# Kernel optimization log

Hardware: AMD Instinct MI355X
Metric: run time of the kernel (lower is better)

Reference implementation:

```python
import jax, jax.numpy as jnp
import numpy as np

N, E, D = 10000, 320000, 256


def setup_inputs() -> dict:
    key = jax.random.key(0)
    ks = jax.random.split(key, 6)
    return {
        "event_emb": jax.random.normal(ks[0], (N, D), jnp.float32),
        "edge_index": jax.random.randint(ks[1], (2, E), 0, N),
        # GCNConv params (weight [D,D] + bias)
        "W1": jax.random.normal(ks[2], (D, D), jnp.float32) / np.sqrt(D).astype(np.float32),
        "b1": jnp.zeros((D,), jnp.float32),
        # GATConv params (shared lin for src/dst when in==out, heads=1, concat=False)
        "W2": jax.random.normal(ks[3], (D, D), jnp.float32) / np.sqrt(D).astype(np.float32),
        "att_src": jax.random.normal(ks[4], (D,), jnp.float32) / np.sqrt(D).astype(np.float32),
        "att_dst": jax.random.normal(ks[5], (D,), jnp.float32) / np.sqrt(D).astype(np.float32),
        "b2": jnp.zeros((D,), jnp.float32),
    }


def _add_self_loops(src, dst, n):
    loop = jnp.arange(n, dtype=src.dtype)
    return jnp.concatenate([src, loop]), jnp.concatenate([dst, loop])


def _gcn_conv(x, W, b, src, dst, n):
    # PyG GCNConv: D^{-1/2} (A+I) D^{-1/2} X W + b ; self-loops already in src/dst
    xw = x @ W  # [N, D]
    deg = jax.ops.segment_sum(jnp.ones(src.shape[0], x.dtype), dst, num_segments=n)
    dinv = jnp.where(deg > 0, jax.lax.rsqrt(deg), 0.0)
    norm = dinv[src] * dinv[dst]  # [E+N]
    agg = jax.ops.segment_sum(xw[src] * norm[:, None], dst, num_segments=n)
    return agg + b


def _gat_conv(x, W, a_src, a_dst, b, src, dst, n):
    # PyG GATConv heads=1, concat=False, negative_slope=0.2, add_self_loops=True
    xw = x @ W  # [N, D]
    e = jax.nn.leaky_relu((xw @ a_src)[src] + (xw @ a_dst)[dst], 0.2)  # [E+N]
    # softmax over incoming edges of each destination node
    m = jax.ops.segment_max(e, dst, num_segments=n)
    ex = jnp.exp(e - m[dst])
    s = jax.ops.segment_sum(ex, dst, num_segments=n)
    alpha = ex / (s[dst] + 1e-16)
    agg = jax.ops.segment_sum(alpha[:, None] * xw[src], dst, num_segments=n)
    return agg + b


def reference(event_emb, edge_index, W1, b1, W2, att_src, att_dst, b2):
    n = event_emb.shape[0]
    src, dst = _add_self_loops(edge_index[0], edge_index[1], n)
    x = jax.nn.relu(_gcn_conv(event_emb, W1, b1, src, dst, n))
    x = jax.nn.relu(_gat_conv(x, W2, att_src, att_dst, b2, src, dst, n))
    return x
```

## Files before the change

kernel.cpp:

```cpp
#include <hip/hip_runtime.h>
#include <hip/hip_fp16.h>

#define D 256
#define UN 8
#define CAP 64

typedef __attribute__((ext_vector_type(4))) _Float16 half4v;

__device__ __forceinline__ float leaky(float x) { return x > 0.f ? x : 0.2f * x; }

__global__ void fill_direct(const int* __restrict__ src, const int* __restrict__ dst, int E,
                            int* __restrict__ cnt, int* __restrict__ csr) {
    int e = blockIdx.x * blockDim.x + threadIdx.x;
    if (e < E) {
        int d = dst[e];
        int pos = atomicAdd(&cnt[d], 1);
        if (pos < CAP) csr[d * CAP + pos] = src[e];
    }
}

__global__ void gemm1_pre(const float* __restrict__ A, const float* __restrict__ B,
                          const int* __restrict__ cnt, _Float16* __restrict__ C, int M) {
    __shared__ float As[16][64];
    __shared__ float Bs[16][64];
    int t = threadIdx.x;
    int tx = t & 15, ty = t >> 4;
    int m0 = blockIdx.x << 6;
    int n0 = blockIdx.y << 6;
    int ar = t >> 2;
    int ak = (t & 3) << 2;
    int br = t >> 4;
    int bc = (t & 15) << 2;
    int arow = m0 + ar;
    if (arow >= M) arow = M - 1;
    float acc[4][4] = {};
    for (int k0 = 0; k0 < D; k0 += 16) {
        float4 av = *(const float4*)(A + (size_t)arow * D + k0 + ak);
        float4 bv = *(const float4*)(B + (size_t)(k0 + br) * D + n0 + bc);
        __syncthreads();
        As[ak + 0][ar] = av.x;
        As[ak + 1][ar] = av.y;
        As[ak + 2][ar] = av.z;
        As[ak + 3][ar] = av.w;
        *(float4*)(&Bs[br][bc]) = bv;
        __syncthreads();
#pragma unroll
        for (int kk = 0; kk < 16; kk++) {
            float4 a = *(const float4*)(&As[kk][ty << 2]);
            float4 b = *(const float4*)(&Bs[kk][tx << 2]);
            acc[0][0] += a.x * b.x; acc[0][1] += a.x * b.y; acc[0][2] += a.x * b.z; acc[0][3] += a.x * b.w;
            acc[1][0] += a.y * b.x; acc[1][1] += a.y * b.y; acc[1][2] += a.y * b.z; acc[1][3] += a.y * b.w;
            acc[2][0] += a.z * b.x; acc[2][1] += a.z * b.y; acc[2][2] += a.z * b.z; acc[2][3] += a.z * b.w;
            acc[3][0] += a.w * b.x; acc[3][1] += a.w * b.y; acc[3][2] += a.w * b.z; acc[3][3] += a.w * b.w;
        }
    }
#pragma unroll
    for (int i = 0; i < 4; i++) {
        int m = m0 + (ty << 2) + i;
        if (m < M) {
            float sc = rsqrtf((float)cnt[m] + 1.0f);
            half4v v = {(_Float16)(acc[i][0] * sc), (_Float16)(acc[i][1] * sc),
                        (_Float16)(acc[i][2] * sc), (_Float16)(acc[i][3] * sc)};
            *(half4v*)(C + (size_t)m * D + n0 + (tx << 2)) = v;
        }
    }
}

__global__ void gemm2_att(const float* __restrict__ A, const float* __restrict__ B,
                          const float* __restrict__ atS, const float* __restrict__ atD,
                          float* __restrict__ asrc, float* __restrict__ adst,
                          _Float16* __restrict__ C, int M) {
    __shared__ float As[16][64];
    __shared__ float Bs[16][64];
    int t = threadIdx.x;
    int tx = t & 15, ty = t >> 4;
    int m0 = blockIdx.x << 6;
    int n0 = blockIdx.y << 6;
    int ar = t >> 2;
    int ak = (t & 3) << 2;
    int br = t >> 4;
    int bc = (t & 15) << 2;
    int arow = m0 + ar;
    if (arow >= M) arow = M - 1;
    float acc[4][4] = {};
    for (int k0 = 0; k0 < D; k0 += 16) {
        float4 av = *(const float4*)(A + (size_t)arow * D + k0 + ak);
        float4 bv = *(const float4*)(B + (size_t)(k0 + br) * D + n0 + bc);
        __syncthreads();
        As[ak + 0][ar] = av.x;
        As[ak + 1][ar] = av.y;
        As[ak + 2][ar] = av.z;
        As[ak + 3][ar] = av.w;
        *(float4*)(&Bs[br][bc]) = bv;
        __syncthreads();
#pragma unroll
        for (int kk = 0; kk < 16; kk++) {
            float4 a = *(const float4*)(&As[kk][ty << 2]);
            float4 b = *(const float4*)(&Bs[kk][tx << 2]);
            acc[0][0] += a.x * b.x; acc[0][1] += a.x * b.y; acc[0][2] += a.x * b.z; acc[0][3] += a.x * b.w;
            acc[1][0] += a.y * b.x; acc[1][1] += a.y * b.y; acc[1][2] += a.y * b.z; acc[1][3] += a.y * b.w;
            acc[2][0] += a.z * b.x; acc[2][1] += a.z * b.y; acc[2][2] += a.z * b.z; acc[2][3] += a.z * b.w;
            acc[3][0] += a.w * b.x; acc[3][1] += a.w * b.y; acc[3][2] += a.w * b.z; acc[3][3] += a.w * b.w;
        }
    }
    float4 as4 = *(const float4*)(atS + n0 + (tx << 2));
    float4 ad4 = *(const float4*)(atD + n0 + (tx << 2));
#pragma unroll
    for (int i = 0; i < 4; i++) {
        int m = m0 + (ty << 2) + i;
        float ps = acc[i][0] * as4.x + acc[i][1] * as4.y + acc[i][2] * as4.z + acc[i][3] * as4.w;
        float pd = acc[i][0] * ad4.x + acc[i][1] * ad4.y + acc[i][2] * ad4.z + acc[i][3] * ad4.w;
#pragma unroll
        for (int off = 1; off < 16; off <<= 1) {
            ps += __shfl_xor(ps, off);
            pd += __shfl_xor(pd, off);
        }
        if (m < M) {
            half4v v = {(_Float16)acc[i][0], (_Float16)acc[i][1],
                        (_Float16)acc[i][2], (_Float16)acc[i][3]};
            *(half4v*)(C + (size_t)m * D + n0 + (tx << 2)) = v;
            if (tx == 0) {
                atomicAdd(&asrc[m], ps);
                atomicAdd(&adst[m], pd);
            }
        }
    }
}

__global__ void gcn_agg(const _Float16* __restrict__ xw1h, const int* __restrict__ csr,
                        const int* __restrict__ cnt, const float* __restrict__ b1,
                        float* __restrict__ x1, int n) {
    int node = (blockIdx.x << 2) + (threadIdx.x >> 6);
    if (node >= n) return;
    int lane = threadIdx.x & 63;
    float ax[UN][4];
#pragma unroll
    for (int j = 0; j < UN; j++) { ax[j][0] = ax[j][1] = ax[j][2] = ax[j][3] = 0.f; }
    {
        half4v v = ((const half4v*)(xw1h + (size_t)node * D))[lane];
        ax[0][0] = (float)v[0]; ax[0][1] = (float)v[1];
        ax[0][2] = (float)v[2]; ax[0][3] = (float)v[3];
    }
    int c = cnt[node];
    int deg = c < CAP ? c : CAP;
    int beg = node * CAP, end = beg + deg;
    int e = beg;
    for (; e + UN <= end; e += UN) {
        int s[UN];
#pragma unroll
        for (int j = 0; j < UN; j++) s[j] = csr[e + j];
#pragma unroll
        for (int j = 0; j < UN; j++) {
            half4v u = ((const half4v*)(xw1h + (size_t)s[j] * D))[lane];
            ax[j][0] += (float)u[0]; ax[j][1] += (float)u[1];
            ax[j][2] += (float)u[2]; ax[j][3] += (float)u[3];
        }
    }
    for (; e < end; e++) {
        int s = csr[e];
        half4v u = ((const half4v*)(xw1h + (size_t)s * D))[lane];
        ax[0][0] += (float)u[0]; ax[0][1] += (float)u[1];
        ax[0][2] += (float)u[2]; ax[0][3] += (float)u[3];
    }
    float a0 = 0.f, a1 = 0.f, a2 = 0.f, a3 = 0.f;
#pragma unroll
    for (int j = 0; j < UN; j++) { a0 += ax[j][0]; a1 += ax[j][1]; a2 += ax[j][2]; a3 += ax[j][3]; }
    float dd = rsqrtf((float)c + 1.0f);
    int c4 = lane * 4;
    float4 bb = *(const float4*)(b1 + c4);
    a0 = a0 * dd + bb.x; a1 = a1 * dd + bb.y; a2 = a2 * dd + bb.z; a3 = a3 * dd + bb.w;
    a0 = a0 > 0.f ? a0 : 0.f;
    a1 = a1 > 0.f ? a1 : 0.f;
    a2 = a2 > 0.f ? a2 : 0.f;
    a3 = a3 > 0.f ? a3 : 0.f;
    *(float4*)(x1 + (size_t)node * D + c4) = make_float4(a0, a1, a2, a3);
}

__global__ void gat_agg(const _Float16* __restrict__ xw2, const int* __restrict__ csr,
                        const int* __restrict__ cnt, const float* __restrict__ asrc,
                        const float* __restrict__ adst, const float* __restrict__ b2,
                        float* __restrict__ out, int n) {
    int node = (blockIdx.x << 2) + (threadIdx.x >> 6);
    if (node >= n) return;
    int lane = threadIdx.x & 63;
    float ad = adst[node];
    float e_self = leaky(asrc[node] + ad);
    float mj[UN], sj[UN], aj[UN][4];
#pragma unroll
    for (int j = 0; j < UN; j++) {
        mj[j] = -1e30f; sj[j] = 0.f;
        aj[j][0] = aj[j][1] = aj[j][2] = aj[j][3] = 0.f;
    }
    {
        half4v v = ((const half4v*)(xw2 + (size_t)node * D))[lane];
        mj[0] = e_self; sj[0] = 1.0f;
        aj[0][0] = (float)v[0]; aj[0][1] = (float)v[1];
        aj[0][2] = (float)v[2]; aj[0][3] = (float)v[3];
    }
    int c = cnt[node];
    int deg = c < CAP ? c : CAP;
    int beg = node * CAP, end = beg + deg;
    int e = beg;
    for (; e + UN <= end; e += UN) {
        int s[UN];
        float ev[UN];
#pragma unroll
        for (int j = 0; j < UN; j++) s[j] = csr[e + j];
#pragma unroll
        for (int j = 0; j < UN; j++) ev[j] = leaky(asrc[s[j]] + ad);
#pragma unroll
        for (int j = 0; j < UN; j++) {
            half4v u = ((const half4v*)(xw2 + (size_t)s[j] * D))[lane];
            float nm = mj[j] > ev[j] ? mj[j] : ev[j];
            float f = __expf(mj[j] - nm);
            float w = __expf(ev[j] - nm);
            mj[j] = nm;
            sj[j] = sj[j] * f + w;
            aj[j][0] = aj[j][0] * f + (float)u[0] * w;
            aj[j][1] = aj[j][1] * f + (float)u[1] * w;
            aj[j][2] = aj[j][2] * f + (float)u[2] * w;
            aj[j][3] = aj[j][3] * f + (float)u[3] * w;
        }
    }
    for (; e < end; e++) {
        int s = csr[e];
        float ev = leaky(asrc[s] + ad);
        half4v u = ((const half4v*)(xw2 + (size_t)s * D))[lane];
        float nm = mj[0] > ev ? mj[0] : ev;
        float f = __expf(mj[0] - nm);
        float w = __expf(ev - nm);
        mj[0] = nm;
        sj[0] = sj[0] * f + w;
        aj[0][0] = aj[0][0] * f + (float)u[0] * w;
        aj[0][1] = aj[0][1] * f + (float)u[1] * w;
        aj[0][2] = aj[0][2] * f + (float)u[2] * w;
        aj[0][3] = aj[0][3] * f + (float)u[3] * w;
    }
    float M = mj[0];
#pragma unroll
    for (int j = 1; j < UN; j++) M = M > mj[j] ? M : mj[j];
    float a0 = 0.f, a1 = 0.f, a2 = 0.f, a3 = 0.f, ssum = 0.f;
#pragma unroll
    for (int j = 0; j < UN; j++) {
        float f = __expf(mj[j] - M);
        ssum += sj[j] * f;
        a0 += aj[j][0] * f; a1 += aj[j][1] * f;
        a2 += aj[j][2] * f; a3 += aj[j][3] * f;
    }
    float inv = 1.0f / (ssum + 1e-16f);
    int c4 = lane * 4;
    float4 bb = *(const float4*)(b2 + c4);
    float r0 = a0 * inv + bb.x;
    float r1 = a1 * inv + bb.y;
    float r2 = a2 * inv + bb.z;
    float r3 = a3 * inv + bb.w;
    r0 = r0 > 0.f ? r0 : 0.f;
    r1 = r1 > 0.f ? r1 : 0.f;
    r2 = r2 > 0.f ? r2 : 0.f;
    r3 = r3 > 0.f ? r3 : 0.f;
    *(float4*)(out + (size_t)node * D + c4) = make_float4(r0, r1, r2, r3);
}


extern "C" void kernel_launch(void* const* d_in, const int* in_sizes, int n_in,
                              void* d_out, int out_size, void* d_ws, size_t ws_size,
                              hipStream_t stream) {
    const float* emb = (const float*)d_in[0];
    const int*   ei  = (const int*)d_in[1];
    const float* W1  = (const float*)d_in[2];
    const float* b1  = (const float*)d_in[3];
    const float* W2  = (const float*)d_in[4];
    const float* atS = (const float*)d_in[5];
    const float* atD = (const float*)d_in[6];
    const float* b2  = (const float*)d_in[7];

    int n = in_sizes[0] / D;
    int E = in_sizes[1] / 2;
    const int* src = ei;
    const int* dst = ei + E;

    char* w = (char*)d_ws;
    auto alloc = [&](size_t bytes) -> char* {
        char* p = w;
        w += (bytes + 255) & ~(size_t)255;
        return p;
    };
    int*      cnt  = (int*)alloc((size_t)n * 12);
    float*    asrc = (float*)(cnt + n);
    float*    adst = asrc + n;
    int*      csr  = (int*)alloc((size_t)n * CAP * 4);
    _Float16* xw1h = (_Float16*)alloc((size_t)n * D * 2);
    float*    x1   = (float*)alloc((size_t)n * D * 4);
    _Float16* xw2h = xw1h;

    hipMemsetAsync(cnt, 0, (size_t)n * 12, stream);

    int eb = (E + 255) / 256;
    fill_direct<<<eb, 256, 0, stream>>>(src, dst, E, cnt, csr);

    dim3 ggrid((n + 63) / 64, 4);
    gemm1_pre<<<ggrid, 256, 0, stream>>>(emb, W1, cnt, xw1h, n);

    int nb = (n + 3) / 4;
    gcn_agg<<<nb, 256, 0, stream>>>(xw1h, csr, cnt, b1, x1, n);

    gemm2_att<<<ggrid, 256, 0, stream>>>(x1, W2, atS, atD, asrc, adst, xw2h, n);

    gat_agg<<<nb, 256, 0, stream>>>(xw2h, csr, cnt, asrc, adst, b2, (float*)d_out, n);
}
```

Before: 199.9 us.

## Fuse all GNN stages into one cooperative persistent kernel with grid syncs

Replaces the memset and five separate launches with one cooperative kernel. It zeroes the counters, builds the CSR, and runs both GEMMs and both aggregations as grid-stride loops over tiles and node groups, with grid.sync between phases. The aim is to remove per-launch overhead and the gaps between kernels. In exchange, each phase runs on a persistent grid capped at 1024 blocks, which may reduce latency hiding in the gather stages, and each grid barrier has its own cost. The original multi-kernel path stays as a fallback if the cooperative launch fails.

Result: slower. 537.0 us (+168.6%).

```diff
diff --git a/kernel.cpp b/kernel.cpp
--- a/kernel.cpp
+++ b/kernel.cpp
@@ -1,5 +1,8 @@
 #include <hip/hip_runtime.h>
 #include <hip/hip_fp16.h>
+#include <hip/hip_cooperative_groups.h>
+
+namespace cg = cooperative_groups;
 
 #define D 256
 #define UN 8
@@ -9,28 +12,16 @@
 
 __device__ __forceinline__ float leaky(float x) { return x > 0.f ? x : 0.2f * x; }
 
-__global__ void fill_direct(const int* __restrict__ src, const int* __restrict__ dst, int E,
-                            int* __restrict__ cnt, int* __restrict__ csr) {
-    int e = blockIdx.x * blockDim.x + threadIdx.x;
-    if (e < E) {
-        int d = dst[e];
-        int pos = atomicAdd(&cnt[d], 1);
-        if (pos < CAP) csr[d * CAP + pos] = src[e];
-    }
-}
-
-__global__ void gemm1_pre(const float* __restrict__ A, const float* __restrict__ B,
-                          const int* __restrict__ cnt, _Float16* __restrict__ C, int M) {
+
+__device__ void gemm1_tile(const float* __restrict__ A, const float* __restrict__ B,
+                           const int* __restrict__ cnt, _Float16* __restrict__ C,
+                           int M, int bx, int by) {
     __shared__ float As[16][64];
     __shared__ float Bs[16][64];
     int t = threadIdx.x;
     int tx = t & 15, ty = t >> 4;
-    int m0 = blockIdx.x << 6;
-    int n0 = blockIdx.y << 6;
-    int ar = t >> 2;
-    int ak = (t & 3) << 2;
-    int br = t >> 4;
-    int bc = (t & 15) << 2;
+    int m0 = bx << 6, n0 = by << 6;
+    int ar = t >> 2, ak = (t & 3) << 2, br = t >> 4, bc = (t & 15) << 2;
     int arow = m0 + ar;
     if (arow >= M) arow = M - 1;
     float acc[4][4] = {};
@@ -66,20 +57,16 @@
     }
 }
 
-__global__ void gemm2_att(const float* __restrict__ A, const float* __restrict__ B,
-                          const float* __restrict__ atS, const float* __restrict__ atD,
-                          float* __restrict__ asrc, float* __restrict__ adst,
-                          _Float16* __restrict__ C, int M) {
+__device__ void gemm2_tile(const float* __restrict__ A, const float* __restrict__ B,
+                           const float* __restrict__ atS, const float* __restrict__ atD,
+                           float* __restrict__ asrc, float* __restrict__ adst,
+                           _Float16* __restrict__ C, int M, int bx, int by) {
     __shared__ float As[16][64];
     __shared__ float Bs[16][64];
     int t = threadIdx.x;
     int tx = t & 15, ty = t >> 4;
-    int m0 = blockIdx.x << 6;
-    int n0 = blockIdx.y << 6;
-    int ar = t >> 2;
-    int ak = (t & 3) << 2;
-    int br = t >> 4;
-    int bc = (t & 15) << 2;
+    int m0 = bx << 6, n0 = by << 6;
+    int ar = t >> 2, ak = (t & 3) << 2, br = t >> 4, bc = (t & 15) << 2;
     int arow = m0 + ar;
     if (arow >= M) arow = M - 1;
     float acc[4][4] = {};
@@ -127,10 +114,10 @@
     }
 }
 
-__global__ void gcn_agg(const _Float16* __restrict__ xw1h, const int* __restrict__ csr,
-                        const int* __restrict__ cnt, const float* __restrict__ b1,
-                        float* __restrict__ x1, int n) {
-    int node = (blockIdx.x << 2) + (threadIdx.x >> 6);
+__device__ void gcn_group(const _Float16* __restrict__ xw1h, const int* __restrict__ csr,
+                          const int* __restrict__ cnt, const float* __restrict__ b1,
+                          float* __restrict__ x1, int n, int g) {
+    int node = (g << 2) + (threadIdx.x >> 6);
     if (node >= n) return;
     int lane = threadIdx.x & 63;
     float ax[UN][4];
@@ -176,11 +163,11 @@
     *(float4*)(x1 + (size_t)node * D + c4) = make_float4(a0, a1, a2, a3);
 }
 
-__global__ void gat_agg(const _Float16* __restrict__ xw2, const int* __restrict__ csr,
-                        const int* __restrict__ cnt, const float* __restrict__ asrc,
-                        const float* __restrict__ adst, const float* __restrict__ b2,
-                        float* __restrict__ out, int n) {
-    int node = (blockIdx.x << 2) + (threadIdx.x >> 6);
+__device__ void gat_group(const _Float16* __restrict__ xw2, const int* __restrict__ csr,
+                          const int* __restrict__ cnt, const float* __restrict__ asrc,
+                          const float* __restrict__ adst, const float* __restrict__ b2,
+                          float* __restrict__ out, int n, int g) {
+    int node = (g << 2) + (threadIdx.x >> 6);
     if (node >= n) return;
     int lane = threadIdx.x & 63;
     float ad = adst[node];
@@ -261,6 +248,80 @@
     *(float4*)(out + (size_t)node * D + c4) = make_float4(r0, r1, r2, r3);
 }
 
+__global__ __launch_bounds__(256, 4) void fused_all(
+    const float* __restrict__ emb, const int* __restrict__ src, const int* __restrict__ dst,
+    const float* __restrict__ W1, const float* __restrict__ b1, const float* __restrict__ W2,
+    const float* __restrict__ atS, const float* __restrict__ atD, const float* __restrict__ b2,
+    int* cnt, float* asrc, float* adst, int* csr,
+    _Float16* xw1h, float* x1, float* out, int n, int E) {
+    cg::grid_group grid = cg::this_grid();
+    const int nb = gridDim.x;
+    const int tid = blockIdx.x * 256 + threadIdx.x;
+    const int nthr = nb * 256;
+
+    for (int i = tid; i < 3 * n; i += nthr) cnt[i] = 0;
+    grid.sync();
+
+    for (int e = tid; e < E; e += nthr) {
+        int d = dst[e];
+        int pos = atomicAdd(&cnt[d], 1);
+        if (pos < CAP) csr[d * CAP + pos] = src[e];
+    }
+    grid.sync();
+
+    {
+        int tiles = ((n + 63) >> 6) * 4;
+        for (int tl = blockIdx.x; tl < tiles; tl += nb)
+            gemm1_tile(emb, W1, cnt, xw1h, n, tl >> 2, tl & 3);
+    }
+    grid.sync();
+
+    {
+        int groups = (n + 3) >> 2;
+        for (int g = blockIdx.x; g < groups; g += nb)
+            gcn_group(xw1h, csr, cnt, b1, x1, n, g);
+    }
+    grid.sync();
+
+    {
+        int tiles = ((n + 63) >> 6) * 4;
+        for (int tl = blockIdx.x; tl < tiles; tl += nb)
+            gemm2_tile(x1, W2, atS, atD, asrc, adst, xw1h, n, tl >> 2, tl & 3);
+    }
+    grid.sync();
+
+    {
+        int groups = (n + 3) >> 2;
+        for (int g = blockIdx.x; g < groups; g += nb)
+            gat_group(xw1h, csr, cnt, asrc, adst, b2, out, n, g);
+    }
+}
+
+__global__ void k_fill(const int* __restrict__ src, const int* __restrict__ dst, int E,
+                       int* __restrict__ cnt, int* __restrict__ csr) {
+    int e = blockIdx.x * blockDim.x + threadIdx.x;
+    if (e < E) {
+        int d = dst[e];
+        int pos = atomicAdd(&cnt[d], 1);
+        if (pos < CAP) csr[d * CAP + pos] = src[e];
+    }
+}
+__global__ void k_gemm1(const float* A, const float* B, const int* cnt, _Float16* C, int M) {
+    gemm1_tile(A, B, cnt, C, M, blockIdx.x, blockIdx.y);
+}
+__global__ void k_gcn(const _Float16* xw1h, const int* csr, const int* cnt,
+                      const float* b1, float* x1, int n) {
+    gcn_group(xw1h, csr, cnt, b1, x1, n, blockIdx.x);
+}
+__global__ void k_gemm2(const float* A, const float* B, const float* atS, const float* atD,
+                        float* asrc, float* adst, _Float16* C, int M) {
+    gemm2_tile(A, B, atS, atD, asrc, adst, C, M, blockIdx.x, blockIdx.y);
+}
+__global__ void k_gat(const _Float16* xw2, const int* csr, const int* cnt, const float* asrc,
+                      const float* adst, const float* b2, float* out, int n) {
+    gat_group(xw2, csr, cnt, asrc, adst, b2, out, n, blockIdx.x);
+}
+
 
 extern "C" void kernel_launch(void* const* d_in, const int* in_sizes, int n_in,
                               void* d_out, int out_size, void* d_ws, size_t ws_size,
@@ -291,20 +352,35 @@
     int*      csr  = (int*)alloc((size_t)n * CAP * 4);
     _Float16* xw1h = (_Float16*)alloc((size_t)n * D * 2);
     float*    x1   = (float*)alloc((size_t)n * D * 4);
-    _Float16* xw2h = xw1h;
-
-    hipMemsetAsync(cnt, 0, (size_t)n * 12, stream);
-
-    int eb = (E + 255) / 256;
-    fill_direct<<<eb, 256, 0, stream>>>(src, dst, E, cnt, csr);
-
-    dim3 ggrid((n + 63) / 64, 4);
-    gemm1_pre<<<ggrid, 256, 0, stream>>>(emb, W1, cnt, xw1h, n);
-
-    int nb = (n + 3) / 4;
-    gcn_agg<<<nb, 256, 0, stream>>>(xw1h, csr, cnt, b1, x1, n);
-
-    gemm2_att<<<ggrid, 256, 0, stream>>>(x1, W2, atS, atD, asrc, adst, xw2h, n);
-
-    gat_agg<<<nb, 256, 0, stream>>>(xw2h, csr, cnt, asrc, adst, b2, (float*)d_out, n);
-}
+    float*    outp = (float*)d_out;
+
+    int dev = 0;
+    hipGetDevice(&dev);
+    int ncu = 0;
+    hipDeviceGetAttribute(&ncu, hipDeviceAttributeMultiprocessorCount, dev);
+    int maxb = 0;
+    hipOccupancyMaxActiveBlocksPerMultiprocessor(&maxb, fused_all, 256, 0);
+    long capb = (long)maxb * (long)ncu;
+    int grid = (capb < 1) ? 0 : (int)(capb < 1024 ? capb : 1024);
+
+    hipError_t rc = hipErrorUnknown;
+    if (grid > 0) {
+        void* args[] = {(void*)&emb, (void*)&src, (void*)&dst, (void*)&W1, (void*)&b1,
+                        (void*)&W2, (void*)&atS, (void*)&atD, (void*)&b2,
+                        (void*)&cnt, (void*)&asrc, (void*)&adst, (void*)&csr,
+                        (void*)&xw1h, (void*)&x1, (void*)&outp, (void*)&n, (void*)&E};
+        rc = hipLaunchCooperativeKernel((const void*)fused_all, dim3(grid), dim3(256),
+                                        args, 0, stream);
+    }
+    if (rc != hipSuccess) {
+        hipMemsetAsync(cnt, 0, (size_t)n * 12, stream);
+        int eb = (E + 255) / 256;
+        k_fill<<<eb, 256, 0, stream>>>(src, dst, E, cnt, csr);
+        dim3 ggrid((n + 63) / 64, 4);
+        k_gemm1<<<ggrid, 256, 0, stream>>>(emb, W1, cnt, xw1h, n);
+        int nb = (n + 3) / 4;
+        k_gcn<<<nb, 256, 0, stream>>>(xw1h, csr, cnt, b1, x1, n);
+        k_gemm2<<<ggrid, 256, 0, stream>>>(x1, W2, atS, atD, asrc, adst, xw1h, n);
+        k_gat<<<nb, 256, 0, stream>>>(xw1h, csr, cnt, asrc, adst, b2, outp, n);
+    }
+}
```

## Replace FP32 SIMT GEMMs with split-FP16 MFMA matrix-core GEMMs

Applied to the files above, without the earlier changes.

Both dense projections move from a shared-memory tiled FP32 FMA kernel to MFMA 16x16x32 f16 instructions, one 16x16 output tile per wave. Each FP32 operand is split into high and low halves, and three MFMA products approximate FP32 accuracy. Operands are loaded straight from global memory with no shared-memory staging, so the strided column loads of W and reloads across tiles may cost bandwidth. The grid assumes n is a multiple of 16, because the row bound check was dropped.

Result: slower. 205.9 us (+3.0%).

```diff
diff --git a/kernel.cpp b/kernel.cpp
--- a/kernel.cpp
+++ b/kernel.cpp
@@ -6,6 +6,8 @@
 #define CAP 64
 
 typedef __attribute__((ext_vector_type(4))) _Float16 half4v;
+typedef __attribute__((ext_vector_type(8))) _Float16 half8v;
+typedef __attribute__((ext_vector_type(4))) float floatx4;
 
 __device__ __forceinline__ float leaky(float x) { return x > 0.f ? x : 0.2f * x; }
 
@@ -19,110 +21,102 @@
     }
 }
 
-__global__ void gemm1_pre(const float* __restrict__ A, const float* __restrict__ B,
-                          const int* __restrict__ cnt, _Float16* __restrict__ C, int M) {
-    __shared__ float As[16][64];
-    __shared__ float Bs[16][64];
-    int t = threadIdx.x;
-    int tx = t & 15, ty = t >> 4;
-    int m0 = blockIdx.x << 6;
-    int n0 = blockIdx.y << 6;
-    int ar = t >> 2;
-    int ak = (t & 3) << 2;
-    int br = t >> 4;
-    int bc = (t & 15) << 2;
-    int arow = m0 + ar;
-    if (arow >= M) arow = M - 1;
-    float acc[4][4] = {};
-    for (int k0 = 0; k0 < D; k0 += 16) {
-        float4 av = *(const float4*)(A + (size_t)arow * D + k0 + ak);
-        float4 bv = *(const float4*)(B + (size_t)(k0 + br) * D + n0 + bc);
-        __syncthreads();
-        As[ak + 0][ar] = av.x;
-        As[ak + 1][ar] = av.y;
-        As[ak + 2][ar] = av.z;
-        As[ak + 3][ar] = av.w;
-        *(float4*)(&Bs[br][bc]) = bv;
-        __syncthreads();
-#pragma unroll
-        for (int kk = 0; kk < 16; kk++) {
-            float4 a = *(const float4*)(&As[kk][ty << 2]);
-            float4 b = *(const float4*)(&Bs[kk][tx << 2]);
-            acc[0][0] += a.x * b.x; acc[0][1] += a.x * b.y; acc[0][2] += a.x * b.z; acc[0][3] += a.x * b.w;
-            acc[1][0] += a.y * b.x; acc[1][1] += a.y * b.y; acc[1][2] += a.y * b.z; acc[1][3] += a.y * b.w;
-            acc[2][0] += a.z * b.x; acc[2][1] += a.z * b.y; acc[2][2] += a.z * b.z; acc[2][3] += a.z * b.w;
-            acc[3][0] += a.w * b.x; acc[3][1] += a.w * b.y; acc[3][2] += a.w * b.z; acc[3][3] += a.w * b.w;
-        }
-    }
-#pragma unroll
-    for (int i = 0; i < 4; i++) {
-        int m = m0 + (ty << 2) + i;
-        if (m < M) {
-            float sc = rsqrtf((float)cnt[m] + 1.0f);
-            half4v v = {(_Float16)(acc[i][0] * sc), (_Float16)(acc[i][1] * sc),
-                        (_Float16)(acc[i][2] * sc), (_Float16)(acc[i][3] * sc)};
-            *(half4v*)(C + (size_t)m * D + n0 + (tx << 2)) = v;
-        }
-    }
-}
-
-__global__ void gemm2_att(const float* __restrict__ A, const float* __restrict__ B,
-                          const float* __restrict__ atS, const float* __restrict__ atD,
-                          float* __restrict__ asrc, float* __restrict__ adst,
-                          _Float16* __restrict__ C, int M) {
-    __shared__ float As[16][64];
-    __shared__ float Bs[16][64];
-    int t = threadIdx.x;
-    int tx = t & 15, ty = t >> 4;
-    int m0 = blockIdx.x << 6;
-    int n0 = blockIdx.y << 6;
-    int ar = t >> 2;
-    int ak = (t & 3) << 2;
-    int br = t >> 4;
-    int bc = (t & 15) << 2;
-    int arow = m0 + ar;
-    if (arow >= M) arow = M - 1;
-    float acc[4][4] = {};
-    for (int k0 = 0; k0 < D; k0 += 16) {
-        float4 av = *(const float4*)(A + (size_t)arow * D + k0 + ak);
-        float4 bv = *(const float4*)(B + (size_t)(k0 + br) * D + n0 + bc);
-        __syncthreads();
-        As[ak + 0][ar] = av.x;
-        As[ak + 1][ar] = av.y;
-        As[ak + 2][ar] = av.z;
-        As[ak + 3][ar] = av.w;
-        *(float4*)(&Bs[br][bc]) = bv;
-        __syncthreads();
-#pragma unroll
-        for (int kk = 0; kk < 16; kk++) {
-            float4 a = *(const float4*)(&As[kk][ty << 2]);
-            float4 b = *(const float4*)(&Bs[kk][tx << 2]);
-            acc[0][0] += a.x * b.x; acc[0][1] += a.x * b.y; acc[0][2] += a.x * b.z; acc[0][3] += a.x * b.w;
-            acc[1][0] += a.y * b.x; acc[1][1] += a.y * b.y; acc[1][2] += a.y * b.z; acc[1][3] += a.y * b.w;
-            acc[2][0] += a.z * b.x; acc[2][1] += a.z * b.y; acc[2][2] += a.z * b.z; acc[2][3] += a.z * b.w;
-            acc[3][0] += a.w * b.x; acc[3][1] += a.w * b.y; acc[3][2] += a.w * b.z; acc[3][3] += a.w * b.w;
-        }
-    }
-    float4 as4 = *(const float4*)(atS + n0 + (tx << 2));
-    float4 ad4 = *(const float4*)(atD + n0 + (tx << 2));
-#pragma unroll
-    for (int i = 0; i < 4; i++) {
-        int m = m0 + (ty << 2) + i;
-        float ps = acc[i][0] * as4.x + acc[i][1] * as4.y + acc[i][2] * as4.z + acc[i][3] * as4.w;
-        float pd = acc[i][0] * ad4.x + acc[i][1] * ad4.y + acc[i][2] * ad4.z + acc[i][3] * ad4.w;
+__global__ void gemm1_mfma(const float* __restrict__ A, const float* __restrict__ W,
+                           const int* __restrict__ cnt, _Float16* __restrict__ C, int M) {
+    int wave = threadIdx.x >> 6;
+    int lane = threadIdx.x & 63;
+    int mt = (blockIdx.x << 2) + wave;
+    if (mt * 16 >= M) return;
+    int m0 = mt << 4, n0 = blockIdx.y << 4;
+    int col = lane & 15, quad = lane >> 4;
+    const float* arow = A + (size_t)(m0 + col) * D + quad * 8;
+    const float* bbase = W + n0 + col + (size_t)quad * 8 * D;
+    floatx4 acc0 = {0.f, 0.f, 0.f, 0.f};
+    floatx4 acc1 = {0.f, 0.f, 0.f, 0.f};
+    floatx4 acc2 = {0.f, 0.f, 0.f, 0.f};
+#pragma unroll
+    for (int k0 = 0; k0 < D; k0 += 32) {
+        float av[8], bv[8];
+        *(float4*)(av + 0) = *(const float4*)(arow + k0);
+        *(float4*)(av + 4) = *(const float4*)(arow + k0 + 4);
+#pragma unroll
+        for (int j = 0; j < 8; j++) bv[j] = bbase[(size_t)(k0 + j) * D];
+        half8v ah, al, bh, bl;
+#pragma unroll
+        for (int j = 0; j < 8; j++) {
+            _Float16 h = (_Float16)av[j];
+            ah[j] = h;
+            al[j] = (_Float16)(av[j] - (float)h);
+            _Float16 g = (_Float16)bv[j];
+            bh[j] = g;
+            bl[j] = (_Float16)(bv[j] - (float)g);
+        }
+        acc0 = __builtin_amdgcn_mfma_f32_16x16x32_f16(ah, bh, acc0, 0, 0, 0);
+        acc1 = __builtin_amdgcn_mfma_f32_16x16x32_f16(ah, bl, acc1, 0, 0, 0);
+        acc2 = __builtin_amdgcn_mfma_f32_16x16x32_f16(al, bh, acc2, 0, 0, 0);
+    }
+#pragma unroll
+    for (int r = 0; r < 4; r++) {
+        int row = m0 + quad * 4 + r;
+        float v = acc0[r] + acc1[r] + acc2[r];
+        float sc = rsqrtf((float)cnt[row] + 1.0f);
+        C[(size_t)row * D + n0 + col] = (_Float16)(v * sc);
+    }
+}
+
+__global__ void gemm2_mfma(const float* __restrict__ A, const float* __restrict__ W,
+                           const float* __restrict__ atS, const float* __restrict__ atD,
+                           float* __restrict__ asrc, float* __restrict__ adst,
+                           _Float16* __restrict__ C, int M) {
+    int wave = threadIdx.x >> 6;
+    int lane = threadIdx.x & 63;
+    int mt = (blockIdx.x << 2) + wave;
+    if (mt * 16 >= M) return;
+    int m0 = mt << 4, n0 = blockIdx.y << 4;
+    int col = lane & 15, quad = lane >> 4;
+    const float* arow = A + (size_t)(m0 + col) * D + quad * 8;
+    const float* bbase = W + n0 + col + (size_t)quad * 8 * D;
+    floatx4 acc0 = {0.f, 0.f, 0.f, 0.f};
+    floatx4 acc1 = {0.f, 0.f, 0.f, 0.f};
+    floatx4 acc2 = {0.f, 0.f, 0.f, 0.f};
+#pragma unroll
+    for (int k0 = 0; k0 < D; k0 += 32) {
+        float av[8], bv[8];
+        *(float4*)(av + 0) = *(const float4*)(arow + k0);
+        *(float4*)(av + 4) = *(const float4*)(arow + k0 + 4);
+#pragma unroll
+        for (int j = 0; j < 8; j++) bv[j] = bbase[(size_t)(k0 + j) * D];
+        half8v ah, al, bh, bl;
+#pragma unroll
+        for (int j = 0; j < 8; j++) {
+            _Float16 h = (_Float16)av[j];
+            ah[j] = h;
+            al[j] = (_Float16)(av[j] - (float)h);
+            _Float16 g = (_Float16)bv[j];
+            bh[j] = g;
+            bl[j] = (_Float16)(bv[j] - (float)g);
+        }
+        acc0 = __builtin_amdgcn_mfma_f32_16x16x32_f16(ah, bh, acc0, 0, 0, 0);
+        acc1 = __builtin_amdgcn_mfma_f32_16x16x32_f16(ah, bl, acc1, 0, 0, 0);
+        acc2 = __builtin_amdgcn_mfma_f32_16x16x32_f16(al, bh, acc2, 0, 0, 0);
+    }
+    float s_at = atS[n0 + col];
+    float d_at = atD[n0 + col];
+#pragma unroll
+    for (int r = 0; r < 4; r++) {
+        int row = m0 + quad * 4 + r;
+        float v = acc0[r] + acc1[r] + acc2[r];
+        C[(size_t)row * D + n0 + col] = (_Float16)v;
+        float ps = v * s_at;
+        float pd = v * d_at;
 #pragma unroll
         for (int off = 1; off < 16; off <<= 1) {
             ps += __shfl_xor(ps, off);
             pd += __shfl_xor(pd, off);
         }
-        if (m < M) {
-            half4v v = {(_Float16)acc[i][0], (_Float16)acc[i][1],
-                        (_Float16)acc[i][2], (_Float16)acc[i][3]};
-            *(half4v*)(C + (size_t)m * D + n0 + (tx << 2)) = v;
-            if (tx == 0) {
-                atomicAdd(&asrc[m], ps);
-                atomicAdd(&adst[m], pd);
-            }
+        if (col == 0) {
+            atomicAdd(&asrc[row], ps);
+            atomicAdd(&adst[row], pd);
         }
     }
 }
@@ -298,13 +292,13 @@
     int eb = (E + 255) / 256;
     fill_direct<<<eb, 256, 0, stream>>>(src, dst, E, cnt, csr);
 
-    dim3 ggrid((n + 63) / 64, 4);
-    gemm1_pre<<<ggrid, 256, 0, stream>>>(emb, W1, cnt, xw1h, n);
+    dim3 mg((n / 16 + 3) / 4, 16);
+    gemm1_mfma<<<mg, 256, 0, stream>>>(emb, W1, cnt, xw1h, n);
 
     int nb = (n + 3) / 4;
     gcn_agg<<<nb, 256, 0, stream>>>(xw1h, csr, cnt, b1, x1, n);
 
-    gemm2_att<<<ggrid, 256, 0, stream>>>(x1, W2, atS, atD, asrc, adst, xw2h, n);
+    gemm2_mfma<<<mg, 256, 0, stream>>>(x1, W2, atS, atD, asrc, adst, xw2h, n);
 
     gat_agg<<<nb, 256, 0, stream>>>(xw2h, csr, cnt, asrc, adst, b2, (float*)d_out, n);
 }
```
